# Performance work log

Hardware: AMD Instinct MI355X
Metric: run time of the kernel (lower is better)

## Reference

```python
import jax, jax.numpy as jnp
import numpy as np

NUM_HEADS = 8


def setup_inputs() -> dict:
    key = jax.random.key(0)
    ks = jax.random.split(key, 5)
    B, C, H, W = 2, 256, 64, 64
    # 0.02 scaling keeps logits in a sane range so softmax is not one-hot
    return {
        "x": jax.random.normal(ks[0], (B, C, H, W), dtype=jnp.float32),
        "w_qkv": jax.random.normal(ks[1], (3 * C, C), dtype=jnp.float32) * 0.02,
        "b_qkv": jax.random.normal(ks[2], (3 * C,), dtype=jnp.float32) * 0.02,
        "w_proj": jax.random.normal(ks[3], (C, C), dtype=jnp.float32) * 0.02,
        "b_proj": jax.random.normal(ks[4], (C,), dtype=jnp.float32) * 0.02,
    }


def reference(x, w_qkv, b_qkv, w_proj, b_proj):
    B, C, H, W = x.shape
    N = H * W
    h = NUM_HEADS
    d = C // h
    # 1x1 conv == per-pixel linear: (B,C,H,W) -> (B,3C,H,W)
    qkv = jnp.einsum('oc,bchw->bohw', w_qkv, x) + b_qkv[None, :, None, None]
    qkv = qkv.reshape(B, 3, h, d, N)
    # q,k,v: (B, h, N, d)
    q = jnp.swapaxes(qkv[:, 0], -2, -1)
    k = jnp.swapaxes(qkv[:, 1], -2, -1)
    v = jnp.swapaxes(qkv[:, 2], -2, -1)
    scale = d ** (-0.5)
    attn = jax.nn.softmax(jnp.einsum('bhnd,bhmd->bhnm', q, k) * scale, axis=-1)
    out = jnp.einsum('bhnm,bhmd->bhnd', attn, v)  # (B, h, N, d)
    # faithful to torch: transpose(1,2) -> (B,N,h,d), then row-major reshape to (B,C,H,W)
    out = jnp.swapaxes(out, 1, 2).reshape(B, C, H, W)
    out = jnp.einsum('oc,bchw->bohw', w_proj, out) + b_proj[None, :, None, None]
    return out
```

## Files before the change

### kernel.cpp

```cpp
#include <hip/hip_runtime.h>
#include <hip/hip_bf16.h>


typedef __bf16 bf16;
typedef __bf16 bf16x4 __attribute__((ext_vector_type(4)));
typedef __bf16 bf16x8 __attribute__((ext_vector_type(8)));
typedef float  f32x4  __attribute__((ext_vector_type(4)));
typedef short  s16x4  __attribute__((ext_vector_type(4)));

#if __has_builtin(__builtin_amdgcn_mfma_f32_16x16x16bf16_1k)
#define HAVE_MFMA16 1
#endif

#if __has_builtin(__builtin_amdgcn_exp2f)
#define EXP2(x) __builtin_amdgcn_exp2f(x)
#else
#define EXP2(x) exp2f(x)
#endif

#define NS 4096
#define QSCALE (0.17677669529663687f * 1.4426950408889634f)

static __device__ inline unsigned pack2(float a, float b) {
  union { bf16 h[2]; unsigned u; } v;
  v.h[0] = (bf16)a; v.h[1] = (bf16)b;
  return v.u;
}

__global__ __launch_bounds__(256) void qkv_fused(
    const float* __restrict__ x, const float* __restrict__ w,
    const float* __restrict__ bias,
    bf16* __restrict__ qbuf, bf16* __restrict__ kbuf, bf16* __restrict__ vbuf)
{
  __shared__ bf16 As[64 * 264];
  __shared__ bf16 Bs[64 * 264];
  const int n0 = blockIdx.x * 64, o0 = blockIdx.y * 64, b = blockIdx.z;
  const int t = threadIdx.x;
  const int wv = t >> 6, L = t & 63, quad = L >> 4, lb = L & 15;

  {
    unsigned* A32 = (unsigned*)As;
    const int nj = (t & 15) * 4;
#pragma unroll
    for (int p = 0; p < 8; p++) {
      const int c = p * 32 + (t >> 4) * 2;
      const float* xr = x + ((size_t)(b * 256 + c)) * NS + n0 + nj;
      f32x4 va = *(const f32x4*)xr;
      f32x4 vb = *(const f32x4*)(xr + NS);
#pragma unroll
      for (int i = 0; i < 4; i++)
        A32[(nj + i) * 132 + (c >> 1)] = pack2(va[i], vb[i]);
    }
  }
  {
    const int cj = (t & 15) * 16;
#pragma unroll
    for (int p = 0; p < 4; p++) {
      const int r = p * 16 + (t >> 4);
      const float* wr = w + (size_t)(o0 + r) * 256 + cj;
      f32x4 w0 = *(const f32x4*)wr,       w1 = *(const f32x4*)(wr + 4);
      f32x4 w2 = *(const f32x4*)(wr + 8), w3 = *(const f32x4*)(wr + 12);
      bf16x8 lo, hi;
#pragma unroll
      for (int i = 0; i < 4; i++) {
        lo[i] = (bf16)w0[i]; lo[4 + i] = (bf16)w1[i];
        hi[i] = (bf16)w2[i]; hi[4 + i] = (bf16)w3[i];
      }
      *(bf16x8*)&Bs[r * 264 + cj] = lo;
      *(bf16x8*)&Bs[r * 264 + cj + 8] = hi;
    }
  }
  __syncthreads();

  f32x4 acc[4] = {};
#pragma unroll
  for (int ks = 0; ks < 8; ks++) {
    const bf16x8 bfr = *(const bf16x8*)&Bs[(wv * 16 + lb) * 264 + ks * 32 + quad * 8];
#pragma unroll
    for (int a = 0; a < 4; a++) {
      const bf16x8 afr = *(const bf16x8*)&As[(a * 16 + lb) * 264 + ks * 32 + quad * 8];
      acc[a] = __builtin_amdgcn_mfma_f32_16x16x32_bf16(afr, bfr, acc[a], 0, 0, 0);
    }
  }

  const int comp = o0 >> 8;
  const int o = o0 + wv * 16 + lb;
  const float bv = bias[o];
  if (comp < 2) {
    bf16* dst = (comp == 0) ? qbuf : kbuf;
    const float sc = (comp == 0) ? QSCALE : 1.0f;
    const int hh = (o & 255) >> 5, dd = o & 31;
    const size_t base = ((size_t)b * 8 + hh) * NS;
#pragma unroll
    for (int a = 0; a < 4; a++)
#pragma unroll
      for (int r = 0; r < 4; r++) {
        const int n = n0 + a * 16 + quad * 4 + r;
        dst[(base + n) * 32 + dd] = (bf16)((acc[a][r] + bv) * sc);
      }
  } else {
    __syncthreads();
    bf16* Vt2 = As;
#pragma unroll
    for (int a = 0; a < 4; a++)
#pragma unroll
      for (int r = 0; r < 4; r++)
        Vt2[(wv * 16 + lb) * 72 + a * 16 + quad * 4 + r] = (bf16)(acc[a][r] + bv);
    __syncthreads();
    const int row = t & 63;
    const int o2 = o0 + row;
    const int hh2 = (o2 & 255) >> 5, dd2 = o2 & 31;
    const int hc = (t >> 6) * 16;
    bf16x8 v0 = *(const bf16x8*)&Vt2[row * 72 + hc];
    bf16x8 v1 = *(const bf16x8*)&Vt2[row * 72 + hc + 8];
    bf16* vd = vbuf + (((size_t)b * 8 + hh2) * 32 + dd2) * NS + n0 + hc;
    *(bf16x8*)vd = v0;
    *(bf16x8*)(vd + 8) = v1;
  }
}

#define KS_OFF 0
#define VT_OFF 2560
#define KV_SZ  (2560 + 32 * 72)

__global__ __launch_bounds__(512) void attn_kernel(
    const bf16* __restrict__ qbuf, const bf16* __restrict__ kbuf,
    const bf16* __restrict__ vbuf, bf16* __restrict__ abuf)
{
  __shared__ bf16 KV[2][KV_SZ];
#ifndef HAVE_MFMA16
  __shared__ bf16 Ps[8][16 * 72];
#endif

  const int qb = blockIdx.x;
  const int bh = blockIdx.y;
  const bf16* Q  = qbuf + (size_t)bh * NS * 32;
  const bf16* K  = kbuf + (size_t)bh * NS * 32;
  const bf16* Vt = vbuf + (size_t)bh * 32 * NS;

  const int t = threadIdx.x;
  const int wv = t >> 6, L = t & 63, quad = L >> 4, lb = L & 15;
  const int qrow = qb * 128 + wv * 16;

  const bf16x8 qfrag = *(const bf16x8*)(Q + (size_t)(qrow + lb) * 32 + quad * 8);

  const int u = t & 255;
  const bool kside = t < 256;
  const int soff = kside ? ((u >> 2) * 40 + (u & 3) * 8)
                         : (VT_OFF + (u >> 3) * 72 + (u & 7) * 8);
  const bf16* gsrc = kside ? (K + (size_t)(u >> 2) * 32 + (u & 3) * 8)
                           : (Vt + (size_t)(u >> 3) * NS + (u & 7) * 8);
  const int gstep = kside ? 64 * 32 : 64;

  bf16x8 reg = *(const bf16x8*)gsrc;

  f32x4 oacc0 = {0.f, 0.f, 0.f, 0.f};
  f32x4 oacc1 = {0.f, 0.f, 0.f, 0.f};
  f32x4 oacc2 = {0.f, 0.f, 0.f, 0.f};
  const f32x4 zero4 = {0.f, 0.f, 0.f, 0.f};
#ifdef HAVE_MFMA16
  const s16x4 ones = {(short)0x3F80, (short)0x3F80, (short)0x3F80, (short)0x3F80};
#else
  float l_i = 0.f;
#endif

#pragma unroll 2
  for (int kt = 0; kt < 64; kt++) {
    const int buf = kt & 1;
    *(bf16x8*)&KV[buf][soff] = reg;
    __syncthreads();
    if (kt < 63) reg = *(const bf16x8*)(gsrc + (size_t)(kt + 1) * gstep);

    f32x4 st[4];
#pragma unroll
    for (int bi = 0; bi < 4; bi++) {
      const bf16x8 kf = *(const bf16x8*)&KV[buf][(bi * 16 + lb) * 40 + quad * 8];
      st[bi] = __builtin_amdgcn_mfma_f32_16x16x32_bf16(kf, qfrag, zero4, 0, 0, 0);
    }

#pragma unroll
    for (int bi = 0; bi < 4; bi++)
#pragma unroll
      for (int r = 0; r < 4; r++) st[bi][r] = EXP2(st[bi][r]);

#ifdef HAVE_MFMA16
#pragma unroll
    for (int bi = 0; bi < 4; bi++) {
      bf16x4 pb;
#pragma unroll
      for (int r = 0; r < 4; r++) pb[r] = (bf16)st[bi][r];
      const s16x4 pf = __builtin_bit_cast(s16x4, pb);
      const s16x4 vf0 = __builtin_bit_cast(s16x4,
          *(const bf16x4*)&KV[buf][VT_OFF + lb * 72 + bi * 16 + quad * 4]);
      const s16x4 vf1 = __builtin_bit_cast(s16x4,
          *(const bf16x4*)&KV[buf][VT_OFF + (16 + lb) * 72 + bi * 16 + quad * 4]);
      oacc0 = __builtin_amdgcn_mfma_f32_16x16x16bf16_1k(pf, vf0, oacc0, 0, 0, 0);
      oacc1 = __builtin_amdgcn_mfma_f32_16x16x16bf16_1k(pf, vf1, oacc1, 0, 0, 0);
      oacc2 = __builtin_amdgcn_mfma_f32_16x16x16bf16_1k(pf, ones, oacc2, 0, 0, 0);
    }
#else
    {
      float ls = 0.f;
#pragma unroll
      for (int bi = 0; bi < 4; bi++)
#pragma unroll
        for (int r = 0; r < 4; r++) ls += st[bi][r];
      l_i += ls;
      bf16* P = &Ps[wv][0];
#pragma unroll
      for (int bi = 0; bi < 4; bi++) {
        bf16x4 pk;
#pragma unroll
        for (int r = 0; r < 4; r++) pk[r] = (bf16)st[bi][r];
        *(bf16x4*)&P[lb * 72 + bi * 16 + quad * 4] = pk;
      }
#pragma unroll
      for (int ch = 0; ch < 2; ch++) {
        const bf16x8 pf  = *(const bf16x8*)&P[lb * 72 + ch * 32 + quad * 8];
        const bf16x8 vf0 = *(const bf16x8*)&KV[buf][VT_OFF + lb * 72 + ch * 32 + quad * 8];
        const bf16x8 vf1 = *(const bf16x8*)&KV[buf][VT_OFF + (16 + lb) * 72 + ch * 32 + quad * 8];
        oacc0 = __builtin_amdgcn_mfma_f32_16x16x32_bf16(pf, vf0, oacc0, 0, 0, 0);
        oacc1 = __builtin_amdgcn_mfma_f32_16x16x32_bf16(pf, vf1, oacc1, 0, 0, 0);
      }
    }
#endif
  }

  const int b_ = bh >> 3;
  const int hh = bh & 7;
#ifndef HAVE_MFMA16
  float lf = l_i;
  lf += __shfl_xor(lf, 16);
  lf += __shfl_xor(lf, 32);
#endif
#pragma unroll
  for (int r = 0; r < 4; r++) {
#ifdef HAVE_MFMA16
    const float lr = oacc2[r];
#else
    const float lr = __shfl(lf, (quad << 4) | (quad * 4 + r));
#endif
#if __has_builtin(__builtin_amdgcn_rcpf)
    const float inv = __builtin_amdgcn_rcpf(lr);
#else
    const float inv = 1.0f / lr;
#endif
    const int n = qrow + quad * 4 + r;
    bf16* dst = abuf + ((size_t)b_ * NS + n) * 256 + hh * 32;
    dst[lb]      = (bf16)(oacc0[r] * inv);
    dst[16 + lb] = (bf16)(oacc1[r] * inv);
  }
}

__global__ __launch_bounds__(256) void proj_fused(
    const bf16* __restrict__ abuf, const float* __restrict__ w,
    const float* __restrict__ bias, float* __restrict__ out)
{
  __shared__ bf16 As[64 * 264];
  __shared__ bf16 Bs[64 * 264];
  const int ch0 = blockIdx.x * 64, o0 = blockIdx.y * 64;
  const int z = blockIdx.z, b = z >> 4, sHi = z & 15;
  const int t = threadIdx.x;
  const int wv = t >> 6, L = t & 63, quad = L >> 4, lb = L & 15;

  {
    const int cj = (t & 15) * 16;
#pragma unroll
    for (int p = 0; p < 4; p++) {
      const int r = p * 16 + (t >> 4);
      const float* wr = w + (size_t)(o0 + r) * 256 + cj;
      f32x4 w0 = *(const f32x4*)wr,       w1 = *(const f32x4*)(wr + 4);
      f32x4 w2 = *(const f32x4*)(wr + 8), w3 = *(const f32x4*)(wr + 12);
      bf16x8 lo, hi;
#pragma unroll
      for (int i = 0; i < 4; i++) {
        lo[i] = (bf16)w0[i]; lo[4 + i] = (bf16)w1[i];
        hi[i] = (bf16)w2[i]; hi[4 + i] = (bf16)w3[i];
      }
      *(bf16x8*)&As[r * 264 + cj] = lo;
      *(bf16x8*)&As[r * 264 + cj + 8] = hi;
    }
  }
  {
    const int chj = (t & 7) * 8;
#pragma unroll
    for (int p = 0; p < 8; p++) {
      const int c = p * 32 + (t >> 3);
      bf16x8 v = *(const bf16x8*)(abuf +
          ((size_t)b * NS + (size_t)c * 16 + sHi) * 256 + ch0 + chj);
#pragma unroll
      for (int i = 0; i < 8; i++) Bs[(chj + i) * 264 + c] = v[i];
    }
  }
  __syncthreads();

  f32x4 acc[4] = {};
#pragma unroll
  for (int ks = 0; ks < 8; ks++) {
    const bf16x8 bfr = *(const bf16x8*)&Bs[(wv * 16 + lb) * 264 + ks * 32 + quad * 8];
#pragma unroll
    for (int a = 0; a < 4; a++) {
      const bf16x8 afr = *(const bf16x8*)&As[(a * 16 + lb) * 264 + ks * 32 + quad * 8];
      acc[a] = __builtin_amdgcn_mfma_f32_16x16x32_bf16(afr, bfr, acc[a], 0, 0, 0);
    }
  }

  const int ch = ch0 + wv * 16 + lb;
#pragma unroll
  for (int a = 0; a < 4; a++)
#pragma unroll
    for (int r = 0; r < 4; r++) {
      const int o = o0 + a * 16 + quad * 4 + r;
      out[((size_t)b * 256 + o) * NS + sHi * 256 + ch] = acc[a][r] + bias[o];
    }
}

extern "C" void kernel_launch(void* const* d_in, const int* in_sizes, int n_in,
                              void* d_out, int out_size, void* d_ws, size_t ws_size,
                              hipStream_t stream) {
  const float* x      = (const float*)d_in[0];
  const float* w_qkv  = (const float*)d_in[1];
  const float* b_qkv  = (const float*)d_in[2];
  const float* w_proj = (const float*)d_in[3];
  const float* b_proj = (const float*)d_in[4];
  float* out = (float*)d_out;

  char* ws = (char*)d_ws;
  const size_t MB = 1024 * 1024;
  bf16* qbuf = (bf16*)(ws);
  bf16* kbuf = (bf16*)(ws + 4 * MB);
  bf16* vbuf = (bf16*)(ws + 8 * MB);
  bf16* abuf = (bf16*)(ws + 12 * MB);

  qkv_fused<<<dim3(64, 12, 2), 256, 0, stream>>>(x, w_qkv, b_qkv, qbuf, kbuf, vbuf);
  attn_kernel<<<dim3(32, 16), 512, 0, stream>>>(qbuf, kbuf, vbuf, abuf);
  proj_fused<<<dim3(4, 4, 32), 256, 0, stream>>>(abuf, w_proj, b_proj, out);
}
```

Measured before the change: 151.5 us.

## Process two query tiles per wave in attention, halving block threads

The attention kernel now runs 4 waves of 256 threads instead of 8 waves, and each wave handles 32 query rows (two 16-row fragments) instead of 16. Each K fragment and V fragment read from shared memory is reused for two sets of MFMAs, which halves LDS reads per unit of work. Every thread now stages both a K and a V chunk. The cost is more accumulator registers, fewer waves to hide latency, and a heavier load per thread.

```diff
diff --git a/kernel.cpp b/kernel.cpp
--- a/kernel.cpp
+++ b/kernel.cpp
@@ -123,13 +123,13 @@
 #define VT_OFF 2560
 #define KV_SZ  (2560 + 32 * 72)
 
-__global__ __launch_bounds__(512) void attn_kernel(
+__global__ __launch_bounds__(256) void attn_kernel(
     const bf16* __restrict__ qbuf, const bf16* __restrict__ kbuf,
     const bf16* __restrict__ vbuf, bf16* __restrict__ abuf)
 {
   __shared__ bf16 KV[2][KV_SZ];
 #ifndef HAVE_MFMA16
-  __shared__ bf16 Ps[8][16 * 72];
+  __shared__ bf16 Ps[4][16 * 72];
 #endif
 
   const int qb = blockIdx.x;
@@ -140,78 +140,92 @@
 
   const int t = threadIdx.x;
   const int wv = t >> 6, L = t & 63, quad = L >> 4, lb = L & 15;
-  const int qrow = qb * 128 + wv * 16;
-
-  const bf16x8 qfrag = *(const bf16x8*)(Q + (size_t)(qrow + lb) * 32 + quad * 8);
-
-  const int u = t & 255;
-  const bool kside = t < 256;
-  const int soff = kside ? ((u >> 2) * 40 + (u & 3) * 8)
-                         : (VT_OFF + (u >> 3) * 72 + (u & 7) * 8);
-  const bf16* gsrc = kside ? (K + (size_t)(u >> 2) * 32 + (u & 3) * 8)
-                           : (Vt + (size_t)(u >> 3) * NS + (u & 7) * 8);
-  const int gstep = kside ? 64 * 32 : 64;
-
-  bf16x8 reg = *(const bf16x8*)gsrc;
-
-  f32x4 oacc0 = {0.f, 0.f, 0.f, 0.f};
-  f32x4 oacc1 = {0.f, 0.f, 0.f, 0.f};
-  f32x4 oacc2 = {0.f, 0.f, 0.f, 0.f};
+  const int qrow = qb * 128 + wv * 32;
+
+  const bf16x8 qfrag0 = *(const bf16x8*)(Q + (size_t)(qrow + lb) * 32 + quad * 8);
+  const bf16x8 qfrag1 = *(const bf16x8*)(Q + (size_t)(qrow + 16 + lb) * 32 + quad * 8);
+
+  const int koff = (t >> 2) * 40 + (t & 3) * 8;
+  const int voff = VT_OFF + (t >> 3) * 72 + (t & 7) * 8;
+  const bf16* gk = K + (size_t)(t >> 2) * 32 + (t & 3) * 8;
+  const bf16* gv = Vt + (size_t)(t >> 3) * NS + (t & 7) * 8;
+
+  bf16x8 regk = *(const bf16x8*)gk;
+  bf16x8 regv = *(const bf16x8*)gv;
+
+  f32x4 oa0 = {0.f, 0.f, 0.f, 0.f}, oa1 = {0.f, 0.f, 0.f, 0.f};
+  f32x4 oa2 = {0.f, 0.f, 0.f, 0.f}, oa3 = {0.f, 0.f, 0.f, 0.f};
+  f32x4 oa4 = {0.f, 0.f, 0.f, 0.f}, oa5 = {0.f, 0.f, 0.f, 0.f};
   const f32x4 zero4 = {0.f, 0.f, 0.f, 0.f};
 #ifdef HAVE_MFMA16
   const s16x4 ones = {(short)0x3F80, (short)0x3F80, (short)0x3F80, (short)0x3F80};
 #else
-  float l_i = 0.f;
+  float l0_i = 0.f, l1_i = 0.f;
 #endif
 
 #pragma unroll 2
   for (int kt = 0; kt < 64; kt++) {
     const int buf = kt & 1;
-    *(bf16x8*)&KV[buf][soff] = reg;
+    *(bf16x8*)&KV[buf][koff] = regk;
+    *(bf16x8*)&KV[buf][voff] = regv;
     __syncthreads();
-    if (kt < 63) reg = *(const bf16x8*)(gsrc + (size_t)(kt + 1) * gstep);
-
-    f32x4 st[4];
+    if (kt < 63) {
+      regk = *(const bf16x8*)(gk + (size_t)(kt + 1) * (64 * 32));
+      regv = *(const bf16x8*)(gv + (size_t)(kt + 1) * 64);
+    }
+
+    f32x4 st0[4], st1[4];
 #pragma unroll
     for (int bi = 0; bi < 4; bi++) {
       const bf16x8 kf = *(const bf16x8*)&KV[buf][(bi * 16 + lb) * 40 + quad * 8];
-      st[bi] = __builtin_amdgcn_mfma_f32_16x16x32_bf16(kf, qfrag, zero4, 0, 0, 0);
+      st0[bi] = __builtin_amdgcn_mfma_f32_16x16x32_bf16(kf, qfrag0, zero4, 0, 0, 0);
+      st1[bi] = __builtin_amdgcn_mfma_f32_16x16x32_bf16(kf, qfrag1, zero4, 0, 0, 0);
     }
 
 #pragma unroll
     for (int bi = 0; bi < 4; bi++)
 #pragma unroll
-      for (int r = 0; r < 4; r++) st[bi][r] = EXP2(st[bi][r]);
+      for (int r = 0; r < 4; r++) {
+        st0[bi][r] = EXP2(st0[bi][r]);
+        st1[bi][r] = EXP2(st1[bi][r]);
+      }
 
 #ifdef HAVE_MFMA16
 #pragma unroll
     for (int bi = 0; bi < 4; bi++) {
-      bf16x4 pb;
-#pragma unroll
-      for (int r = 0; r < 4; r++) pb[r] = (bf16)st[bi][r];
-      const s16x4 pf = __builtin_bit_cast(s16x4, pb);
+      bf16x4 pb0, pb1;
+#pragma unroll
+      for (int r = 0; r < 4; r++) {
+        pb0[r] = (bf16)st0[bi][r];
+        pb1[r] = (bf16)st1[bi][r];
+      }
+      const s16x4 pf0 = __builtin_bit_cast(s16x4, pb0);
+      const s16x4 pf1 = __builtin_bit_cast(s16x4, pb1);
       const s16x4 vf0 = __builtin_bit_cast(s16x4,
           *(const bf16x4*)&KV[buf][VT_OFF + lb * 72 + bi * 16 + quad * 4]);
       const s16x4 vf1 = __builtin_bit_cast(s16x4,
           *(const bf16x4*)&KV[buf][VT_OFF + (16 + lb) * 72 + bi * 16 + quad * 4]);
-      oacc0 = __builtin_amdgcn_mfma_f32_16x16x16bf16_1k(pf, vf0, oacc0, 0, 0, 0);
-      oacc1 = __builtin_amdgcn_mfma_f32_16x16x16bf16_1k(pf, vf1, oacc1, 0, 0, 0);
-      oacc2 = __builtin_amdgcn_mfma_f32_16x16x16bf16_1k(pf, ones, oacc2, 0, 0, 0);
+      oa0 = __builtin_amdgcn_mfma_f32_16x16x16bf16_1k(pf0, vf0, oa0, 0, 0, 0);
+      oa1 = __builtin_amdgcn_mfma_f32_16x16x16bf16_1k(pf0, vf1, oa1, 0, 0, 0);
+      oa2 = __builtin_amdgcn_mfma_f32_16x16x16bf16_1k(pf0, ones, oa2, 0, 0, 0);
+      oa3 = __builtin_amdgcn_mfma_f32_16x16x16bf16_1k(pf1, vf0, oa3, 0, 0, 0);
+      oa4 = __builtin_amdgcn_mfma_f32_16x16x16bf16_1k(pf1, vf1, oa4, 0, 0, 0);
+      oa5 = __builtin_amdgcn_mfma_f32_16x16x16bf16_1k(pf1, ones, oa5, 0, 0, 0);
     }
 #else
     {
-      float ls = 0.f;
+      float ls0 = 0.f, ls1 = 0.f;
 #pragma unroll
       for (int bi = 0; bi < 4; bi++)
 #pragma unroll
-        for (int r = 0; r < 4; r++) ls += st[bi][r];
-      l_i += ls;
+        for (int r = 0; r < 4; r++) { ls0 += st0[bi][r]; ls1 += st1[bi][r]; }
+      l0_i += ls0; l1_i += ls1;
       bf16* P = &Ps[wv][0];
 #pragma unroll
       for (int bi = 0; bi < 4; bi++) {
         bf16x4 pk;
 #pragma unroll
-        for (int r = 0; r < 4; r++) pk[r] = (bf16)st[bi][r];
+        for (int r = 0; r < 4; r++) pk[r] = (bf16)st0[bi][r];
         *(bf16x4*)&P[lb * 72 + bi * 16 + quad * 4] = pk;
       }
 #pragma unroll
@@ -219,8 +233,23 @@
         const bf16x8 pf  = *(const bf16x8*)&P[lb * 72 + ch * 32 + quad * 8];
         const bf16x8 vf0 = *(const bf16x8*)&KV[buf][VT_OFF + lb * 72 + ch * 32 + quad * 8];
         const bf16x8 vf1 = *(const bf16x8*)&KV[buf][VT_OFF + (16 + lb) * 72 + ch * 32 + quad * 8];
-        oacc0 = __builtin_amdgcn_mfma_f32_16x16x32_bf16(pf, vf0, oacc0, 0, 0, 0);
-        oacc1 = __builtin_amdgcn_mfma_f32_16x16x32_bf16(pf, vf1, oacc1, 0, 0, 0);
+        oa0 = __builtin_amdgcn_mfma_f32_16x16x32_bf16(pf, vf0, oa0, 0, 0, 0);
+        oa1 = __builtin_amdgcn_mfma_f32_16x16x32_bf16(pf, vf1, oa1, 0, 0, 0);
+      }
+#pragma unroll
+      for (int bi = 0; bi < 4; bi++) {
+        bf16x4 pk;
+#pragma unroll
+        for (int r = 0; r < 4; r++) pk[r] = (bf16)st1[bi][r];
+        *(bf16x4*)&P[lb * 72 + bi * 16 + quad * 4] = pk;
+      }
+#pragma unroll
+      for (int ch = 0; ch < 2; ch++) {
+        const bf16x8 pf  = *(const bf16x8*)&P[lb * 72 + ch * 32 + quad * 8];
+        const bf16x8 vf0 = *(const bf16x8*)&KV[buf][VT_OFF + lb * 72 + ch * 32 + quad * 8];
+        const bf16x8 vf1 = *(const bf16x8*)&KV[buf][VT_OFF + (16 + lb) * 72 + ch * 32 + quad * 8];
+        oa3 = __builtin_amdgcn_mfma_f32_16x16x32_bf16(pf, vf0, oa3, 0, 0, 0);
+        oa4 = __builtin_amdgcn_mfma_f32_16x16x32_bf16(pf, vf1, oa4, 0, 0, 0);
       }
     }
 #endif
@@ -228,28 +257,45 @@
 
   const int b_ = bh >> 3;
   const int hh = bh & 7;
-#ifndef HAVE_MFMA16
-  float lf = l_i;
-  lf += __shfl_xor(lf, 16);
-  lf += __shfl_xor(lf, 32);
-#endif
+#ifdef HAVE_MFMA16
 #pragma unroll
   for (int r = 0; r < 4; r++) {
-#ifdef HAVE_MFMA16
-    const float lr = oacc2[r];
-#else
-    const float lr = __shfl(lf, (quad << 4) | (quad * 4 + r));
-#endif
 #if __has_builtin(__builtin_amdgcn_rcpf)
-    const float inv = __builtin_amdgcn_rcpf(lr);
-#else
-    const float inv = 1.0f / lr;
-#endif
-    const int n = qrow + quad * 4 + r;
-    bf16* dst = abuf + ((size_t)b_ * NS + n) * 256 + hh * 32;
-    dst[lb]      = (bf16)(oacc0[r] * inv);
-    dst[16 + lb] = (bf16)(oacc1[r] * inv);
-  }
+    const float inv0 = __builtin_amdgcn_rcpf(oa2[r]);
+    const float inv1 = __builtin_amdgcn_rcpf(oa5[r]);
+#else
+    const float inv0 = 1.0f / oa2[r];
+    const float inv1 = 1.0f / oa5[r];
+#endif
+    const int n0_ = qrow + quad * 4 + r;
+    const int n1_ = qrow + 16 + quad * 4 + r;
+    bf16* dst0 = abuf + ((size_t)b_ * NS + n0_) * 256 + hh * 32;
+    bf16* dst1 = abuf + ((size_t)b_ * NS + n1_) * 256 + hh * 32;
+    dst0[lb]      = (bf16)(oa0[r] * inv0);
+    dst0[16 + lb] = (bf16)(oa1[r] * inv0);
+    dst1[lb]      = (bf16)(oa3[r] * inv1);
+    dst1[16 + lb] = (bf16)(oa4[r] * inv1);
+  }
+#else
+  float lf0 = l0_i, lf1 = l1_i;
+  lf0 += __shfl_xor(lf0, 16); lf0 += __shfl_xor(lf0, 32);
+  lf1 += __shfl_xor(lf1, 16); lf1 += __shfl_xor(lf1, 32);
+#pragma unroll
+  for (int r = 0; r < 4; r++) {
+    const float lr0 = __shfl(lf0, (quad << 4) | (quad * 4 + r));
+    const float lr1 = __shfl(lf1, (quad << 4) | (quad * 4 + r));
+    const float inv0 = 1.0f / lr0;
+    const float inv1 = 1.0f / lr1;
+    const int n0_ = qrow + quad * 4 + r;
+    const int n1_ = qrow + 16 + quad * 4 + r;
+    bf16* dst0 = abuf + ((size_t)b_ * NS + n0_) * 256 + hh * 32;
+    bf16* dst1 = abuf + ((size_t)b_ * NS + n1_) * 256 + hh * 32;
+    dst0[lb]      = (bf16)(oa0[r] * inv0);
+    dst0[16 + lb] = (bf16)(oa1[r] * inv0);
+    dst1[lb]      = (bf16)(oa3[r] * inv1);
+    dst1[16 + lb] = (bf16)(oa4[r] * inv1);
+  }
+#endif
 }
 
 __global__ __launch_bounds__(256) void proj_fused(
@@ -333,6 +379,6 @@
   bf16* abuf = (bf16*)(ws + 12 * MB);
 
   qkv_fused<<<dim3(64, 12, 2), 256, 0, stream>>>(x, w_qkv, b_qkv, qbuf, kbuf, vbuf);
-  attn_kernel<<<dim3(32, 16), 512, 0, stream>>>(qbuf, kbuf, vbuf, abuf);
+  attn_kernel<<<dim3(32, 16), 256, 0, stream>>>(qbuf, kbuf, vbuf, abuf);
   proj_fused<<<dim3(4, 4, 32), 256, 0, stream>>>(abuf, w_proj, b_proj, out);
 }
```

After: 158.5 us. 1.05x slower.
